# Optimization experiments

Measured on AMD Instinct MI355X. Metric: run time of the kernel, lower is better.

## Reference

```python
import jax, jax.numpy as jnp
import numpy as np

EMBED_DIM = 1024
NUM_HEADS = 16
HEAD_DIM = EMBED_DIM // NUM_HEADS


def setup_inputs() -> dict:
    key = jax.random.key(0)
    ks = jax.random.split(key, 9)
    B, S, D = 4, 2048, EMBED_DIM
    scale = 1.0 / np.sqrt(D)
    inp = {
        "x": jax.random.normal(ks[0], (B, S, D), dtype=jnp.float32),
        "wq": jax.random.normal(ks[1], (D, D), dtype=jnp.float32) * scale,
        "bq": jnp.zeros((D,), dtype=jnp.float32),
        "wk": jax.random.normal(ks[2], (D, D), dtype=jnp.float32) * scale,
        "bk": jnp.zeros((D,), dtype=jnp.float32),
        "wv": jax.random.normal(ks[3], (D, D), dtype=jnp.float32) * scale,
        "bv": jnp.zeros((D,), dtype=jnp.float32),
        "wo": jax.random.normal(ks[4], (D, D), dtype=jnp.float32) * scale,
        "bo": jnp.zeros((D,), dtype=jnp.float32),
    }
    return inp


def reference(x, wq, bq, wk, bk, wv, bv, wo, bo):
    B, S, D = x.shape
    H, Hd = NUM_HEADS, HEAD_DIM

    def split_heads(t):
        # [B, S, D] -> [B, H, S, Hd]
        return t.reshape(B, S, H, Hd).transpose(0, 2, 1, 3)

    q = split_heads(x @ wq.T + bq)
    k = split_heads(x @ wk.T + bk)
    v = split_heads(x @ wv.T + bv)

    scores = jnp.einsum("bhqd,bhkd->bhqk", q, k) / jnp.sqrt(jnp.float32(Hd))
    attn = jax.nn.softmax(scores, axis=-1)
    out = jnp.einsum("bhqk,bhkd->bhqd", attn, v)  # [B, H, S, Hd]
    out = out.transpose(0, 2, 1, 3).reshape(B, S, D)
    return out @ wo.T + bo
```

## Files before the change

### kernel.cpp

```cpp
#include <hip/hip_runtime.h>
#include <hip/hip_bf16.h>
#include <hip/hip_fp16.h>

typedef _Float16 f16;
typedef f16 f16x8 __attribute__((ext_vector_type(8)));
typedef f16 f16x4 __attribute__((ext_vector_type(4)));
typedef f16 f16x2 __attribute__((ext_vector_type(2)));
typedef float f32x4 __attribute__((ext_vector_type(4)));
typedef float f32x16 __attribute__((ext_vector_type(16)));
typedef unsigned int u32x4 __attribute__((ext_vector_type(4)));
typedef unsigned int u32x2 __attribute__((ext_vector_type(2)));

#define MFMA16(a, b, c) __builtin_amdgcn_mfma_f32_16x16x32_f16(a, b, c, 0, 0, 0)
#define MFMA32(a, b, c) __builtin_amdgcn_mfma_f32_32x32x16_f16(a, b, c, 0, 0, 0)

constexpr int BB = 4, SS = 2048, DD = 1024, HH = 16, HDIM = 64;
constexpr int MM = BB * SS;
constexpr float QSCALE = 0.125f * 1.44269504088896340736f;


__device__ __forceinline__ void gl_lds16(const void* g, void* l) {
  __builtin_amdgcn_global_load_lds((const __attribute__((address_space(1))) void*)g,
                                   (__attribute__((address_space(3))) void*)l, 16, 0, 0);
}

__global__ __launch_bounds__(256) void cvt_all_kernel(const float* __restrict__ x,
                                                      const float* __restrict__ w0,
                                                      const float* __restrict__ w1,
                                                      const float* __restrict__ w2,
                                                      const float* __restrict__ w3,
                                                      f16* xh, f16* o0, f16* o1,
                                                      f16* o2, f16* o3) {
  int bid = blockIdx.x;
  const float* in; f16* out; int idx;
  if (bid < MM * DD / 4 / 256) {
    in = x; out = xh; idx = bid * 256 + threadIdx.x;
  } else {
    int wb = bid - MM * DD / 4 / 256;
    int which = wb >> 10;
    in = which == 0 ? w0 : which == 1 ? w1 : which == 2 ? w2 : w3;
    out = which == 0 ? o0 : which == 1 ? o1 : which == 2 ? o2 : o3;
    idx = (wb & 1023) * 256 + threadIdx.x;
  }
  f32x4 v = reinterpret_cast<const f32x4*>(in)[idx];
  f16x4 o;
  o[0] = (f16)v[0]; o[1] = (f16)v[1]; o[2] = (f16)v[2]; o[3] = (f16)v[3];
  reinterpret_cast<f16x4*>(out)[idx] = o;
}

__device__ __forceinline__ int swz(int row, int slot) {
  return row * 64 + ((slot ^ (row & 7)) << 3);
}

__global__ __launch_bounds__(256) void qkv_kernel(const f16* __restrict__ A,
                                                  const f16* __restrict__ Wq,
                                                  const f16* __restrict__ Wk,
                                                  const f16* __restrict__ Wv,
                                                  const float* __restrict__ bq,
                                                  const float* __restrict__ bk,
                                                  const float* __restrict__ bv,
                                                  f16* __restrict__ Qo,
                                                  f16* __restrict__ Ko,
                                                  f16* __restrict__ Vo) {
  constexpr int K = 1024;
  __shared__ __align__(16) char smem_raw[128 * 136 * 2];
  f16* As = (f16*)smem_raw;
  f16* Ws = As + 128 * 64;

  const int mat = blockIdx.x >> 3;
  const f16* W = mat == 0 ? Wq : (mat == 1 ? Wk : Wv);
  const float* bias = mat == 0 ? bq : (mat == 1 ? bk : bv);
  const float scale = mat == 0 ? QSCALE : 1.0f;

  const int tid = threadIdx.x;
  const int m0 = blockIdx.y * 128, n0 = (blockIdx.x & 7) * 128;
  const int w = tid >> 6, lane = tid & 63;
  const int wm = (w >> 1) * 64, wn = (w & 1) * 64;
  const int g = lane >> 4, r = lane & 15;
  const int srow = lane >> 3;
  const int sslot = (lane & 7) ^ srow;

  f32x4 acc[4][4] = {};

  for (int k0 = 0; k0 < K; k0 += 64) {
#pragma unroll
    for (int i = 0; i < 4; ++i) {
      int rbase = w * 32 + i * 8;
      gl_lds16(A + (size_t)(m0 + rbase + srow) * K + k0 + sslot * 8, As + rbase * 64);
      gl_lds16(W + (size_t)(n0 + rbase + srow) * K + k0 + sslot * 8, Ws + rbase * 64);
    }
    __syncthreads();

#pragma unroll
    for (int ks = 0; ks < 2; ++ks) {
      f16x8 af[4], bf[4];
#pragma unroll
      for (int i = 0; i < 4; ++i) {
        af[i] = *reinterpret_cast<const f16x8*>(As + swz(wm + i * 16 + r, (ks << 2) | g));
        bf[i] = *reinterpret_cast<const f16x8*>(Ws + swz(wn + i * 16 + r, (ks << 2) | g));
      }
#pragma unroll
      for (int i = 0; i < 4; ++i)
#pragma unroll
        for (int j = 0; j < 4; ++j)
          acc[i][j] = MFMA16(af[i], bf[j], acc[i][j]);
    }
    __syncthreads();
  }

  if (mat == 0) {
#pragma unroll
    for (int i = 0; i < 4; ++i)
#pragma unroll
      for (int j = 0; j < 4; ++j)
#pragma unroll
        for (int q = 0; q < 4; ++q) {
          int gm = m0 + wm + i * 16 + g * 4 + q;
          int gn = n0 + wn + j * 16 + r;
          float v = (acc[i][j][q] + bias[gn]) * scale;
          int b = gm >> 11, s = gm & 2047;
          int h = gn >> 6, hd = gn & 63;
          Qo[(((size_t)(b * HH + h)) * SS + s) * HDIM + hd] = (f16)v;
        }
  } else if (mat == 1) {
#pragma unroll
    for (int i = 0; i < 4; ++i)
#pragma unroll
      for (int j = 0; j < 4; ++j)
#pragma unroll
        for (int q = 0; q < 4; ++q) {
          int gm = m0 + wm + i * 16 + g * 4 + q;
          int gn = n0 + wn + j * 16 + r;
          float v = acc[i][j][q] + bias[gn];
          int b = gm >> 11, s = gm & 2047;
          int h = gn >> 6, hd = gn & 63;
          int tile = s >> 6, row = s & 63, slot = hd >> 3, w8 = hd & 7;
          size_t off = ((((size_t)(b * HH + h) * 32 + tile) * 8 + slot) * 64 + row) * 8 + w8;
          Ko[off] = (f16)v;
        }
  } else {
    __syncthreads();
    f16* T = (f16*)smem_raw;
#pragma unroll
    for (int i = 0; i < 4; ++i)
#pragma unroll
      for (int j = 0; j < 4; ++j)
#pragma unroll
        for (int q = 0; q < 4; ++q) {
          int ml = wm + i * 16 + g * 4 + q;
          int nl = wn + j * 16 + r;
          T[nl * 136 + ml] = (f16)(acc[i][j][q] + bias[n0 + nl]);
        }
    __syncthreads();
    const int b = m0 >> 11, sbase = m0 & 2047;
#pragma unroll
    for (int it = 0; it < 8; ++it) {
      int cid = it * 256 + tid;
      int hd_l = cid & 127, sl = (cid >> 7) & 7, tl = cid >> 10;
      u32x4 v = *reinterpret_cast<const u32x4*>(T + hd_l * 136 + tl * 64 + sl * 8);
      int gn = n0 + hd_l, h = gn >> 6, hd = gn & 63;
      int tile = (sbase >> 6) + tl;
      size_t off = ((((size_t)(b * HH + h) * 32 + tile) * 8 + sl) * 64 + hd) * 8;
      *reinterpret_cast<u32x4*>(Vo + off) = v;
    }
  }
}

__global__ __launch_bounds__(256) void oproj_kernel(const f16* __restrict__ A,
                                                    const f16* __restrict__ W,
                                                    const float* __restrict__ bias,
                                                    float* __restrict__ Out) {
  constexpr int K = 1024, N = 1024;
  __shared__ __align__(16) f16 As[128 * 64];
  __shared__ __align__(16) f16 Ws[128 * 64];

  const int tid = threadIdx.x;
  const int m0 = blockIdx.y * 128, n0 = blockIdx.x * 128;
  const int w = tid >> 6, lane = tid & 63;
  const int wm = (w >> 1) * 64, wn = (w & 1) * 64;
  const int g = lane >> 4, r = lane & 15;
  const int srow = lane >> 3;
  const int sslot = (lane & 7) ^ srow;

  f32x4 acc[4][4] = {};

  for (int k0 = 0; k0 < K; k0 += 64) {
#pragma unroll
    for (int i = 0; i < 4; ++i) {
      int rbase = w * 32 + i * 8;
      gl_lds16(A + (size_t)(m0 + rbase + srow) * K + k0 + sslot * 8, As + rbase * 64);
      gl_lds16(W + (size_t)(n0 + rbase + srow) * K + k0 + sslot * 8, Ws + rbase * 64);
    }
    __syncthreads();

#pragma unroll
    for (int ks = 0; ks < 2; ++ks) {
      f16x8 af[4], bf[4];
#pragma unroll
      for (int i = 0; i < 4; ++i) {
        af[i] = *reinterpret_cast<const f16x8*>(As + swz(wm + i * 16 + r, (ks << 2) | g));
        bf[i] = *reinterpret_cast<const f16x8*>(Ws + swz(wn + i * 16 + r, (ks << 2) | g));
      }
#pragma unroll
      for (int i = 0; i < 4; ++i)
#pragma unroll
        for (int j = 0; j < 4; ++j)
          acc[i][j] = MFMA16(af[i], bf[j], acc[i][j]);
    }
    __syncthreads();
  }

#pragma unroll
  for (int i = 0; i < 4; ++i)
#pragma unroll
    for (int j = 0; j < 4; ++j)
#pragma unroll
      for (int q = 0; q < 4; ++q) {
        int gm = m0 + wm + i * 16 + g * 4 + q;
        int gn = n0 + wn + j * 16 + r;
        Out[(size_t)gm * N + gn] = acc[i][j][q] + bias[gn];
      }
}

__global__ __launch_bounds__(256, 4) void attn_kernel(const f16* __restrict__ Q,
                                                      const f16* __restrict__ K,
                                                      const f16* __restrict__ Vt,
                                                      f16* __restrict__ AO) {
  __shared__ __align__(16) f16 Kls[2][8 * 512];
  __shared__ __align__(16) f16 Vls[2][8 * 512];
  __shared__ __align__(16) float Lw[4][32];

  const int tid = threadIdx.x;
  const int w = tid >> 6, lane = tid & 63;
  const int q31 = lane & 31;
  const int h = lane >> 5;
  const int bh = blockIdx.y;
  const int q0 = blockIdx.x * 128;

  const f16* Kg = K + (size_t)bh * (SS * HDIM);
  const f16* Vg = Vt + (size_t)bh * (SS * HDIM);
  const int s0 = 2 * w;
  const int rofs = h * 512 + q31 * 8;

  const f16* Qg = Q + ((size_t)bh * SS + q0 + w * 32 + q31) * HDIM + 8 * h;
  f16x8 qf[4];
#pragma unroll
  for (int m = 0; m < 4; ++m)
    qf[m] = *reinterpret_cast<const f16x8*>(Qg + 16 * m);

  f32x16 oacc[2] = {};
  float lsum = 0.f;

#pragma unroll
  for (int i = 0; i < 2; ++i) {
    int s_idx = s0 + i;
    gl_lds16(Kg + (size_t)(s_idx * 64 + lane) * 8, &Kls[0][s_idx * 512]);
    gl_lds16(Vg + (size_t)(s_idx * 64 + lane) * 8, &Vls[0][s_idx * 512]);
  }
  __syncthreads();

  for (int t = 0; t < SS / 64; ++t) {
    const int cur = t & 1;
    if (t < SS / 64 - 1) {
#pragma unroll
      for (int i = 0; i < 2; ++i) {
        int s_idx = s0 + i;
        gl_lds16(Kg + (size_t)((t + 1) * 512 + s_idx * 64 + lane) * 8,
                 &Kls[cur ^ 1][s_idx * 512]);
        gl_lds16(Vg + (size_t)((t + 1) * 512 + s_idx * 64 + lane) * 8,
                 &Vls[cur ^ 1][s_idx * 512]);
      }
    }
    const f16* Kc = &Kls[cur][0];
    const f16* Vc = &Vls[cur][0];

#pragma unroll
    for (int kb = 0; kb < 2; ++kb) {
      f32x16 sacc = {};
      __builtin_amdgcn_s_setprio(1);
#pragma unroll
      for (int m = 0; m < 4; ++m) {
        f16x8 kf = *reinterpret_cast<const f16x8*>(Kc + m * 1024 + kb * 256 + rofs);
        sacc = MFMA32(kf, qf[m], sacc);
      }
      __builtin_amdgcn_s_setprio(0);

      unsigned pk[8];
#pragma unroll
      for (int rp = 0; rp < 4; ++rp)
#pragma unroll
        for (int p = 0; p < 2; ++p) {
          float e0 = __builtin_amdgcn_exp2f(sacc[4 * rp + 2 * p]);
          float e1 = __builtin_amdgcn_exp2f(sacc[4 * rp + 2 * p + 1]);
          pk[2 * rp + p] = __builtin_bit_cast(unsigned, __builtin_amdgcn_cvt_pkrtz(e0, e1));
        }

      f16x2 s01 = __builtin_bit_cast(f16x2, pk[0]) + __builtin_bit_cast(f16x2, pk[1]);
      f16x2 s23 = __builtin_bit_cast(f16x2, pk[2]) + __builtin_bit_cast(f16x2, pk[3]);
      f16x2 s45 = __builtin_bit_cast(f16x2, pk[4]) + __builtin_bit_cast(f16x2, pk[5]);
      f16x2 s67 = __builtin_bit_cast(f16x2, pk[6]) + __builtin_bit_cast(f16x2, pk[7]);
      f16x2 st = (s01 + s23) + (s45 + s67);
      lsum += (float)st[0] + (float)st[1];

#pragma unroll
      for (int jl = 0; jl < 2; ++jl) {
        auto sw0 = __builtin_amdgcn_permlane32_swap(pk[4 * jl + 0], pk[4 * jl + 2], false, false);
        auto sw1 = __builtin_amdgcn_permlane32_swap(pk[4 * jl + 1], pk[4 * jl + 3], false, false);
        u32x4 fw = {(unsigned)sw0[0], (unsigned)sw1[0], (unsigned)sw0[1], (unsigned)sw1[1]};
        f16x8 pa = __builtin_bit_cast(f16x8, fw);
        const int j = 2 * kb + jl;
        __builtin_amdgcn_s_setprio(1);
#pragma unroll
        for (int vb = 0; vb < 2; ++vb) {
          f16x8 vbf = *reinterpret_cast<const f16x8*>(Vc + j * 1024 + vb * 256 + rofs);
          oacc[vb] = MFMA32(pa, vbf, oacc[vb]);
        }
        __builtin_amdgcn_s_setprio(0);
      }
    }
    __syncthreads();
  }

  lsum += __shfl_xor(lsum, 32, 64);
  if (h == 0) Lw[w][q31] = 1.0f / lsum;

  f32x4 li[4];
#pragma unroll
  for (int rq = 0; rq < 4; ++rq)
    li[rq] = *reinterpret_cast<const f32x4*>(&Lw[w][8 * rq + 4 * h]);

  const int b = bh >> 4, head = bh & 15;
  f16* aobase = AO + ((size_t)(b * SS + q0 + 32 * w)) * DD + head * 64 + q31;
#pragma unroll
  for (int vb = 0; vb < 2; ++vb)
#pragma unroll
    for (int reg = 0; reg < 16; ++reg) {
      int q = (reg & 3) + 8 * (reg >> 2) + 4 * h;
      aobase[(size_t)q * DD + 32 * vb] = (f16)(oacc[vb][reg] * li[reg >> 2][reg & 3]);
    }
}

extern "C" void kernel_launch(void* const* d_in, const int* in_sizes, int n_in,
                              void* d_out, int out_size, void* d_ws, size_t ws_size,
                              hipStream_t stream) {
  (void)in_sizes; (void)n_in; (void)out_size; (void)ws_size;
  const float* x  = (const float*)d_in[0];
  const float* wq = (const float*)d_in[1];
  const float* bq = (const float*)d_in[2];
  const float* wk = (const float*)d_in[3];
  const float* bk = (const float*)d_in[4];
  const float* wv = (const float*)d_in[5];
  const float* bv = (const float*)d_in[6];
  const float* wo = (const float*)d_in[7];
  const float* bo = (const float*)d_in[8];
  float* out = (float*)d_out;

  char* ws = (char*)d_ws;
  f16* xh  = (f16*)ws; ws += (size_t)MM * DD * 2;
  f16* wqh = (f16*)ws; ws += (size_t)DD * DD * 2;
  f16* wkh = (f16*)ws; ws += (size_t)DD * DD * 2;
  f16* wvh = (f16*)ws; ws += (size_t)DD * DD * 2;
  f16* woh = (f16*)ws; ws += (size_t)DD * DD * 2;
  f16* Qb  = (f16*)ws; ws += (size_t)MM * DD * 2;
  f16* Kb  = (f16*)ws; ws += (size_t)MM * DD * 2;
  f16* Vtb = (f16*)ws; ws += (size_t)MM * DD * 2;
  f16* AOb = (f16*)ws; ws += (size_t)MM * DD * 2;

  cvt_all_kernel<<<MM * DD / 4 / 256 + 4 * (DD * DD / 4 / 256), 256, 0, stream>>>(
      x, wq, wk, wv, wo, xh, wqh, wkh, wvh, woh);

  qkv_kernel<<<dim3(24, MM / 128), 256, 0, stream>>>(xh, wqh, wkh, wvh, bq, bk, bv, Qb, Kb, Vtb);

  attn_kernel<<<dim3(SS / 128, BB * HH), 256, 0, stream>>>(Qb, Kb, Vtb, AOb);

  oproj_kernel<<<dim3(DD / 128, MM / 128), 256, 0, stream>>>(AOb, woh, bo, out);
}
```

Baseline: 197.1 us.

## Double attention query tile per wave and swizzle block order for L2 locality

The attention kernel now handles 64 query rows per wave (256 per block), so each K/V fragment loaded from LDS feeds two MFMA chains and K/V traffic per query is halved. Launch bounds drop to 2 blocks per SM to make room for the extra registers. All three GEMM-like kernels switch to 1D grids with a swizzled block-to-tile mapping, so that adjacent blocks (likely placed on different XCDs) share operand rows and columns in cache. The trade-off is higher register pressure and fewer resident waves in attention, plus half as many attention blocks.

```diff
diff --git a/kernel.cpp b/kernel.cpp
--- a/kernel.cpp
+++ b/kernel.cpp
@@ -67,13 +67,17 @@
   f16* As = (f16*)smem_raw;
   f16* Ws = As + 128 * 64;
 
-  const int mat = blockIdx.x >> 3;
+  const int p = blockIdx.x;
+  const int bx = (p >> 3) % 24;
+  const int by = (p & 7) + 8 * ((p >> 3) / 24);
+
+  const int mat = bx >> 3;
   const f16* W = mat == 0 ? Wq : (mat == 1 ? Wk : Wv);
   const float* bias = mat == 0 ? bq : (mat == 1 ? bk : bv);
   const float scale = mat == 0 ? QSCALE : 1.0f;
 
   const int tid = threadIdx.x;
-  const int m0 = blockIdx.y * 128, n0 = (blockIdx.x & 7) * 128;
+  const int m0 = by * 128, n0 = (bx & 7) * 128;
   const int w = tid >> 6, lane = tid & 63;
   const int wm = (w >> 1) * 64, wn = (w & 1) * 64;
   const int g = lane >> 4, r = lane & 15;
@@ -174,8 +178,12 @@
   __shared__ __align__(16) f16 As[128 * 64];
   __shared__ __align__(16) f16 Ws[128 * 64];
 
+  const int p = blockIdx.x;
+  const int bx = (p >> 3) & 7;
+  const int by = (p & 7) | ((p >> 6) << 3);
+
   const int tid = threadIdx.x;
-  const int m0 = blockIdx.y * 128, n0 = blockIdx.x * 128;
+  const int m0 = by * 128, n0 = bx * 128;
   const int w = tid >> 6, lane = tid & 63;
   const int wm = (w >> 1) * 64, wn = (w & 1) * 64;
   const int g = lane >> 4, r = lane & 15;
@@ -222,34 +230,38 @@
       }
 }
 
-__global__ __launch_bounds__(256, 4) void attn_kernel(const f16* __restrict__ Q,
+__global__ __launch_bounds__(256, 2) void attn_kernel(const f16* __restrict__ Q,
                                                       const f16* __restrict__ K,
                                                       const f16* __restrict__ Vt,
                                                       f16* __restrict__ AO) {
   __shared__ __align__(16) f16 Kls[2][8 * 512];
   __shared__ __align__(16) f16 Vls[2][8 * 512];
-  __shared__ __align__(16) float Lw[4][32];
+  __shared__ __align__(16) float Lw[4][64];
+
+  const int p = blockIdx.x;
+  const int qx = (p >> 3) & 7;
+  const int bh = (p & 7) | ((p >> 6) << 3);
+  const int q0 = qx * 256;
 
   const int tid = threadIdx.x;
   const int w = tid >> 6, lane = tid & 63;
   const int q31 = lane & 31;
   const int h = lane >> 5;
-  const int bh = blockIdx.y;
-  const int q0 = blockIdx.x * 128;
-
   const f16* Kg = K + (size_t)bh * (SS * HDIM);
   const f16* Vg = Vt + (size_t)bh * (SS * HDIM);
   const int s0 = 2 * w;
   const int rofs = h * 512 + q31 * 8;
 
-  const f16* Qg = Q + ((size_t)bh * SS + q0 + w * 32 + q31) * HDIM + 8 * h;
-  f16x8 qf[4];
-#pragma unroll
-  for (int m = 0; m < 4; ++m)
-    qf[m] = *reinterpret_cast<const f16x8*>(Qg + 16 * m);
-
-  f32x16 oacc[2] = {};
-  float lsum = 0.f;
+  const f16* Qg = Q + ((size_t)bh * SS + q0 + w * 64 + q31) * HDIM + 8 * h;
+  f16x8 qf[2][4];
+#pragma unroll
+  for (int f = 0; f < 2; ++f)
+#pragma unroll
+    for (int m = 0; m < 4; ++m)
+      qf[f][m] = *reinterpret_cast<const f16x8*>(Qg + f * 32 * HDIM + 16 * m);
+
+  f32x16 oacc[2][2] = {};
+  float lsum0 = 0.f, lsum1 = 0.f;
 
 #pragma unroll
   for (int i = 0; i < 2; ++i) {
@@ -276,44 +288,63 @@
 
 #pragma unroll
     for (int kb = 0; kb < 2; ++kb) {
-      f32x16 sacc = {};
+      f32x16 sc0 = {}, sc1 = {};
       __builtin_amdgcn_s_setprio(1);
 #pragma unroll
       for (int m = 0; m < 4; ++m) {
         f16x8 kf = *reinterpret_cast<const f16x8*>(Kc + m * 1024 + kb * 256 + rofs);
-        sacc = MFMA32(kf, qf[m], sacc);
+        sc0 = MFMA32(kf, qf[0][m], sc0);
+        sc1 = MFMA32(kf, qf[1][m], sc1);
       }
       __builtin_amdgcn_s_setprio(0);
 
-      unsigned pk[8];
+      unsigned pk0[8], pk1[8];
 #pragma unroll
       for (int rp = 0; rp < 4; ++rp)
 #pragma unroll
-        for (int p = 0; p < 2; ++p) {
-          float e0 = __builtin_amdgcn_exp2f(sacc[4 * rp + 2 * p]);
-          float e1 = __builtin_amdgcn_exp2f(sacc[4 * rp + 2 * p + 1]);
-          pk[2 * rp + p] = __builtin_bit_cast(unsigned, __builtin_amdgcn_cvt_pkrtz(e0, e1));
+        for (int pp = 0; pp < 2; ++pp) {
+          float a0 = __builtin_amdgcn_exp2f(sc0[4 * rp + 2 * pp]);
+          float a1 = __builtin_amdgcn_exp2f(sc0[4 * rp + 2 * pp + 1]);
+          pk0[2 * rp + pp] = __builtin_bit_cast(unsigned, __builtin_amdgcn_cvt_pkrtz(a0, a1));
+          float b0 = __builtin_amdgcn_exp2f(sc1[4 * rp + 2 * pp]);
+          float b1 = __builtin_amdgcn_exp2f(sc1[4 * rp + 2 * pp + 1]);
+          pk1[2 * rp + pp] = __builtin_bit_cast(unsigned, __builtin_amdgcn_cvt_pkrtz(b0, b1));
         }
 
-      f16x2 s01 = __builtin_bit_cast(f16x2, pk[0]) + __builtin_bit_cast(f16x2, pk[1]);
-      f16x2 s23 = __builtin_bit_cast(f16x2, pk[2]) + __builtin_bit_cast(f16x2, pk[3]);
-      f16x2 s45 = __builtin_bit_cast(f16x2, pk[4]) + __builtin_bit_cast(f16x2, pk[5]);
-      f16x2 s67 = __builtin_bit_cast(f16x2, pk[6]) + __builtin_bit_cast(f16x2, pk[7]);
-      f16x2 st = (s01 + s23) + (s45 + s67);
-      lsum += (float)st[0] + (float)st[1];
+      {
+        f16x2 s01 = __builtin_bit_cast(f16x2, pk0[0]) + __builtin_bit_cast(f16x2, pk0[1]);
+        f16x2 s23 = __builtin_bit_cast(f16x2, pk0[2]) + __builtin_bit_cast(f16x2, pk0[3]);
+        f16x2 s45 = __builtin_bit_cast(f16x2, pk0[4]) + __builtin_bit_cast(f16x2, pk0[5]);
+        f16x2 s67 = __builtin_bit_cast(f16x2, pk0[6]) + __builtin_bit_cast(f16x2, pk0[7]);
+        f16x2 st = (s01 + s23) + (s45 + s67);
+        lsum0 += (float)st[0] + (float)st[1];
+      }
+      {
+        f16x2 s01 = __builtin_bit_cast(f16x2, pk1[0]) + __builtin_bit_cast(f16x2, pk1[1]);
+        f16x2 s23 = __builtin_bit_cast(f16x2, pk1[2]) + __builtin_bit_cast(f16x2, pk1[3]);
+        f16x2 s45 = __builtin_bit_cast(f16x2, pk1[4]) + __builtin_bit_cast(f16x2, pk1[5]);
+        f16x2 s67 = __builtin_bit_cast(f16x2, pk1[6]) + __builtin_bit_cast(f16x2, pk1[7]);
+        f16x2 st = (s01 + s23) + (s45 + s67);
+        lsum1 += (float)st[0] + (float)st[1];
+      }
 
 #pragma unroll
       for (int jl = 0; jl < 2; ++jl) {
-        auto sw0 = __builtin_amdgcn_permlane32_swap(pk[4 * jl + 0], pk[4 * jl + 2], false, false);
-        auto sw1 = __builtin_amdgcn_permlane32_swap(pk[4 * jl + 1], pk[4 * jl + 3], false, false);
-        u32x4 fw = {(unsigned)sw0[0], (unsigned)sw1[0], (unsigned)sw0[1], (unsigned)sw1[1]};
-        f16x8 pa = __builtin_bit_cast(f16x8, fw);
+        auto a0 = __builtin_amdgcn_permlane32_swap(pk0[4 * jl + 0], pk0[4 * jl + 2], false, false);
+        auto a1 = __builtin_amdgcn_permlane32_swap(pk0[4 * jl + 1], pk0[4 * jl + 3], false, false);
+        u32x4 fa = {(unsigned)a0[0], (unsigned)a1[0], (unsigned)a0[1], (unsigned)a1[1]};
+        f16x8 pa0 = __builtin_bit_cast(f16x8, fa);
+        auto b0 = __builtin_amdgcn_permlane32_swap(pk1[4 * jl + 0], pk1[4 * jl + 2], false, false);
+        auto b1 = __builtin_amdgcn_permlane32_swap(pk1[4 * jl + 1], pk1[4 * jl + 3], false, false);
+        u32x4 fb = {(unsigned)b0[0], (unsigned)b1[0], (unsigned)b0[1], (unsigned)b1[1]};
+        f16x8 pa1 = __builtin_bit_cast(f16x8, fb);
         const int j = 2 * kb + jl;
         __builtin_amdgcn_s_setprio(1);
 #pragma unroll
         for (int vb = 0; vb < 2; ++vb) {
           f16x8 vbf = *reinterpret_cast<const f16x8*>(Vc + j * 1024 + vb * 256 + rofs);
-          oacc[vb] = MFMA32(pa, vbf, oacc[vb]);
+          oacc[0][vb] = MFMA32(pa0, vbf, oacc[0][vb]);
+          oacc[1][vb] = MFMA32(pa1, vbf, oacc[1][vb]);
         }
         __builtin_amdgcn_s_setprio(0);
       }
@@ -321,23 +352,29 @@
     __syncthreads();
   }
 
-  lsum += __shfl_xor(lsum, 32, 64);
-  if (h == 0) Lw[w][q31] = 1.0f / lsum;
-
-  f32x4 li[4];
-#pragma unroll
-  for (int rq = 0; rq < 4; ++rq)
-    li[rq] = *reinterpret_cast<const f32x4*>(&Lw[w][8 * rq + 4 * h]);
+  lsum0 += __shfl_xor(lsum0, 32, 64);
+  lsum1 += __shfl_xor(lsum1, 32, 64);
+  if (h == 0) {
+    Lw[w][q31] = 1.0f / lsum0;
+    Lw[w][32 + q31] = 1.0f / lsum1;
+  }
 
   const int b = bh >> 4, head = bh & 15;
-  f16* aobase = AO + ((size_t)(b * SS + q0 + 32 * w)) * DD + head * 64 + q31;
-#pragma unroll
-  for (int vb = 0; vb < 2; ++vb)
-#pragma unroll
-    for (int reg = 0; reg < 16; ++reg) {
-      int q = (reg & 3) + 8 * (reg >> 2) + 4 * h;
-      aobase[(size_t)q * DD + 32 * vb] = (f16)(oacc[vb][reg] * li[reg >> 2][reg & 3]);
-    }
+#pragma unroll
+  for (int f = 0; f < 2; ++f) {
+    f32x4 li[4];
+#pragma unroll
+    for (int rq = 0; rq < 4; ++rq)
+      li[rq] = *reinterpret_cast<const f32x4*>(&Lw[w][32 * f + 8 * rq + 4 * h]);
+    f16* aobase = AO + ((size_t)(b * SS + q0 + 64 * w + 32 * f)) * DD + head * 64 + q31;
+#pragma unroll
+    for (int vb = 0; vb < 2; ++vb)
+#pragma unroll
+      for (int reg = 0; reg < 16; ++reg) {
+        int q = (reg & 3) + 8 * (reg >> 2) + 4 * h;
+        aobase[(size_t)q * DD + 32 * vb] = (f16)(oacc[f][vb][reg] * li[reg >> 2][reg & 3]);
+      }
+  }
 }
 
 extern "C" void kernel_launch(void* const* d_in, const int* in_sizes, int n_in,
@@ -369,9 +406,9 @@
   cvt_all_kernel<<<MM * DD / 4 / 256 + 4 * (DD * DD / 4 / 256), 256, 0, stream>>>(
       x, wq, wk, wv, wo, xh, wqh, wkh, wvh, woh);
 
-  qkv_kernel<<<dim3(24, MM / 128), 256, 0, stream>>>(xh, wqh, wkh, wvh, bq, bk, bv, Qb, Kb, Vtb);
-
-  attn_kernel<<<dim3(SS / 128, BB * HH), 256, 0, stream>>>(Qb, Kb, Vtb, AOb);
-
-  oproj_kernel<<<dim3(DD / 128, MM / 128), 256, 0, stream>>>(AOb, woh, bo, out);
-}
+  qkv_kernel<<<1536, 256, 0, stream>>>(xh, wqh, wkh, wvh, bq, bk, bv, Qb, Kb, Vtb);
+
+  attn_kernel<<<512, 256, 0, stream>>>(Qb, Kb, Vtb, AOb);
+
+  oproj_kernel<<<512, 256, 0, stream>>>(AOb, woh, bo, out);
+}
```

After: 189.6 us. -3.8%, faster.
